# Kernel optimization log

Measured on AMD Instinct MI355X. Metric: run time of the kernel, lower is better.

## Reference

```python
import jax, jax.numpy as jnp
import numpy as np

# Model dims (see init_kwargs)
B, S = 4, 512
H = 1024            # hidden_size
I = 2816            # expert intermediate_size
E = 8               # num_experts
K = 2               # num_experts_per_tok
IS = 1408           # shared_expert_intermediate_size


def setup_inputs() -> dict:
    key = jax.random.key(0)
    ks = jax.random.split(key, 8)
    def init(k, shape, fan_in):
        return (jax.random.normal(k, shape, jnp.float32) / np.sqrt(fan_in)).astype(jnp.float32)
    return {
        "hidden_states": jax.random.normal(ks[0], (B, S, H), jnp.float32),
        "gate_w": init(ks[1], (H, E), H),          # router Linear (no bias)
        "Wg": init(ks[2], (E, H, I), H),           # per-expert gate_proj
        "Wu": init(ks[3], (E, H, I), H),           # per-expert up_proj
        "Wd": init(ks[4], (E, I, H), I),           # per-expert down_proj
        "Sg": init(ks[5], (H, IS), H),             # shared expert gate_proj
        "Su": init(ks[6], (H, IS), H),             # shared expert up_proj
        "Sd": init(ks[7], (IS, H), IS),            # shared expert down_proj
    }


def reference(hidden_states, gate_w, Wg, Wu, Wd, Sg, Su, Sd):
    b, s, h = hidden_states.shape
    x = hidden_states.reshape(-1, h)                       # [T, H]
    T = x.shape[0]

    # Router: top-k logits, softmax over selected logits only
    logits = x @ gate_w                                    # [T, E]
    top_v, top_i = jax.lax.top_k(logits, K)                # [T, K]
    top_p = jax.nn.softmax(top_v, axis=-1)                 # [T, K]

    # Dense combine weights: combine[t, e] = sum of probs of slots routed to e
    combine = jnp.zeros((T, E), x.dtype).at[
        jnp.arange(T)[:, None], top_i
    ].add(top_p)                                           # [T, E]

    # All-expert SwiGLU (dense, vectorized over experts), then weighted combine
    g = jnp.einsum('th,ehi->tei', x, Wg)                   # [T, E, I]
    u = jnp.einsum('th,ehi->tei', x, Wu)
    d = jnp.einsum('tei,eih->teh', jax.nn.silu(g) * u, Wd) # [T, E, H]
    expert_out = jnp.einsum('te,teh->th', combine, d)      # [T, H]

    # Shared expert (always active)
    shared = (jax.nn.silu(x @ Sg) * (x @ Su)) @ Sd         # [T, H]

    return (expert_out + shared).reshape(b, s, h)
```

## Files before the change

kernel.cpp:

```cpp
#include <hip/hip_runtime.h>
#include <hip/hip_bf16.h>

typedef __bf16 bf16;
typedef __bf16 bf16x4 __attribute__((ext_vector_type(4)));
typedef __bf16 bf16x8 __attribute__((ext_vector_type(8)));
typedef float f32x4 __attribute__((ext_vector_type(4)));

constexpr int T = 2048;
constexpr int HD = 1024;
constexpr int NE = 8;
constexpr int IEXP = 2816;
constexpr int ISH = 1408;
constexpr int NSLOT = T * 2;

typedef __attribute__((address_space(1))) void gvoid;
typedef __attribute__((address_space(3))) void svoid;

__device__ __forceinline__ void gload_lds16(const void* g, void* l) {
  __builtin_amdgcn_global_load_lds((gvoid*)g, (svoid*)l, 16, 0, 0);
}

__global__ __launch_bounds__(256) void k_convert_x(const float* __restrict__ x,
                                                   bf16* __restrict__ xb, int n4) {
  int i = blockIdx.x * blockDim.x + threadIdx.x;
  if (i >= n4) return;
  float4 v = reinterpret_cast<const float4*>(x)[i];
  bf16x4 o; o[0] = (bf16)v.x; o[1] = (bf16)v.y; o[2] = (bf16)v.z; o[3] = (bf16)v.w;
  reinterpret_cast<bf16x4*>(xb)[i] = o;
}

__global__ __launch_bounds__(256) void k_transpose(const float* __restrict__ in,
                                                   bf16* __restrict__ out,
                                                   int Kd, int Nd) {
  __shared__ float tile[32][33];
  int b = blockIdx.z;
  int n0 = blockIdx.x * 32, k0 = blockIdx.y * 32;
  const float* src = in + (size_t)b * Kd * Nd;
  bf16* dst = out + (size_t)b * Kd * Nd;
  int t = threadIdx.x;
  int r = t >> 3, c4 = (t & 7) * 4;
  float4 v = *reinterpret_cast<const float4*>(src + (size_t)(k0 + r) * Nd + n0 + c4);
  tile[r][c4 + 0] = v.x; tile[r][c4 + 1] = v.y; tile[r][c4 + 2] = v.z; tile[r][c4 + 3] = v.w;
  __syncthreads();
  bf16x4 o;
  o[0] = (bf16)tile[c4 + 0][r]; o[1] = (bf16)tile[c4 + 1][r];
  o[2] = (bf16)tile[c4 + 2][r]; o[3] = (bf16)tile[c4 + 3][r];
  *reinterpret_cast<bf16x4*>(dst + (size_t)(n0 + r) * Kd + k0 + c4) = o;
}

__global__ __launch_bounds__(64) void k_router(const float* __restrict__ x,
                                               const float* __restrict__ gw,
                                               int* __restrict__ topi,
                                               float* __restrict__ topp,
                                               int* __restrict__ counts) {
  int t = blockIdx.x;
  int l = threadIdx.x;
  float acc[NE];
  #pragma unroll
  for (int e = 0; e < NE; ++e) acc[e] = 0.f;
  const float* xr = x + (size_t)t * HD;
  for (int i = 0; i < HD / 64; ++i) {
    int h = i * 64 + l;
    float xv = xr[h];
    const float* g = gw + (size_t)h * NE;
    #pragma unroll
    for (int e = 0; e < NE; ++e) acc[e] += xv * g[e];
  }
  #pragma unroll
  for (int e = 0; e < NE; ++e) {
    float v = acc[e];
    #pragma unroll
    for (int s = 32; s; s >>= 1) v += __shfl_xor(v, s);
    acc[e] = v;
  }
  if (l == 0) {
    int i0 = 0; float v0 = acc[0];
    #pragma unroll
    for (int e = 1; e < NE; ++e) if (acc[e] > v0) { v0 = acc[e]; i0 = e; }
    int i1 = -1; float v1 = -1e30f;
    #pragma unroll
    for (int e = 0; e < NE; ++e) if (e != i0 && acc[e] > v1) { v1 = acc[e]; i1 = e; }
    float e1 = expf(v1 - v0);
    float den = 1.f + e1;
    topi[t * 2] = i0; topi[t * 2 + 1] = i1;
    topp[t * 2] = 1.f / den; topp[t * 2 + 1] = e1 / den;
    atomicAdd(&counts[i0], 1);
    atomicAdd(&counts[i1], 1);
  }
}

__global__ void k_scan(const int* __restrict__ counts, int* __restrict__ offs,
                       int* __restrict__ cursor, int* __restrict__ soffs) {
  if (threadIdx.x == 0 && blockIdx.x == 0) {
    int s = 0; offs[0] = 0;
    for (int e = 0; e < NE; ++e) { s += counts[e]; offs[e + 1] = s; cursor[e] = 0; }
    soffs[0] = 0; soffs[1] = T;
  }
}

__global__ __launch_bounds__(64) void k_scatter(const int* __restrict__ topi,
                                                const float* __restrict__ topp,
                                                const int* __restrict__ offs,
                                                int* __restrict__ cursor,
                                                int* __restrict__ rowmap,
                                                float* __restrict__ rowp,
                                                int* __restrict__ slotOf) {
  int t = blockIdx.x * blockDim.x + threadIdx.x;
  if (t >= T) return;
  #pragma unroll
  for (int s = 0; s < 2; ++s) {
    int e = topi[t * 2 + s];
    int pos = offs[e] + atomicAdd(&cursor[e], 1);
    rowmap[pos] = t;
    rowp[pos] = topp[t * 2 + s];
    slotOf[t * 2 + s] = pos;
  }
}

__global__ __launch_bounds__(256) void k_gateup(
    const bf16* __restrict__ A, const int* __restrict__ rowmap,
    const int* __restrict__ offs, const bf16* __restrict__ Bg,
    const bf16* __restrict__ Bu, bf16* __restrict__ outp, int Nd, int Kd) {
  __shared__ alignas(16) bf16 As[128 * 32];
  __shared__ alignas(16) bf16 Bgs[64 * 32];
  __shared__ alignas(16) bf16 Bus[64 * 32];
  const int z = blockIdx.z;
  const int r0 = offs[z], r1 = offs[z + 1];
  const int mbase = r0 + blockIdx.y * 128;
  if (mbase >= r1) return;
  const int n0 = blockIdx.x * 64;
  const int tid = threadIdx.x, wid = tid >> 6, lane = tid & 63;

  const bf16 *aSrc0, *aSrc1;
  {
    int rl0 = wid * 32 + (lane >> 2);
    int g0 = mbase + rl0;      if (g0 >= r1) g0 = r1 - 1;
    int g1 = mbase + rl0 + 16; if (g1 >= r1) g1 = r1 - 1;
    int s0 = rowmap ? rowmap[g0] : g0;
    int s1 = rowmap ? rowmap[g1] : g1;
    aSrc0 = A + (size_t)s0 * Kd + (lane & 3) * 8;
    aSrc1 = A + (size_t)s1 * Kd + (lane & 3) * 8;
  }
  const size_t bstride = (size_t)Nd * Kd;
  const size_t brow = (size_t)(n0 + wid * 16 + (lane >> 2)) * Kd + (lane & 3) * 8;
  const bf16* bgSrc = Bg + (size_t)z * bstride + brow;
  const bf16* buSrc = Bu + (size_t)z * bstride + brow;
  bf16* aDst0 = &As[(wid * 32) * 32];
  bf16* aDst1 = &As[(wid * 32 + 16) * 32];
  bf16* bgDst = &Bgs[(wid * 16) * 32];
  bf16* buDst = &Bus[(wid * 16) * 32];

  f32x4 zz = {0.f, 0.f, 0.f, 0.f};
  f32x4 accg[4][2], accu[4][2];
  #pragma unroll
  for (int m = 0; m < 4; ++m)
    #pragma unroll
    for (int n = 0; n < 2; ++n) { accg[m][n] = zz; accu[m][n] = zz; }

  const int wr = wid >> 1, wc = wid & 1;
  const int frow = lane & 15, fk = (lane >> 4) * 8;

  for (int k0 = 0; k0 < Kd; k0 += 32) {
    gload_lds16(aSrc0 + k0, aDst0);
    gload_lds16(aSrc1 + k0, aDst1);
    gload_lds16(bgSrc + k0, bgDst);
    gload_lds16(buSrc + k0, buDst);
    __syncthreads();
    bf16x8 af[4], bgf[2], buf2[2];
    #pragma unroll
    for (int m = 0; m < 4; ++m)
      af[m] = *reinterpret_cast<const bf16x8*>(&As[(wr * 64 + m * 16 + frow) * 32 + fk]);
    #pragma unroll
    for (int n = 0; n < 2; ++n) {
      bgf[n]  = *reinterpret_cast<const bf16x8*>(&Bgs[(wc * 32 + n * 16 + frow) * 32 + fk]);
      buf2[n] = *reinterpret_cast<const bf16x8*>(&Bus[(wc * 32 + n * 16 + frow) * 32 + fk]);
    }
    #pragma unroll
    for (int m = 0; m < 4; ++m)
      #pragma unroll
      for (int n = 0; n < 2; ++n) {
        accg[m][n] = __builtin_amdgcn_mfma_f32_16x16x32_bf16(af[m], bgf[n],  accg[m][n], 0, 0, 0);
        accu[m][n] = __builtin_amdgcn_mfma_f32_16x16x32_bf16(af[m], buf2[n], accu[m][n], 0, 0, 0);
      }
    __syncthreads();
  }

  #pragma unroll
  for (int m = 0; m < 4; ++m)
    #pragma unroll
    for (int n = 0; n < 2; ++n)
      #pragma unroll
      for (int j = 0; j < 4; ++j) {
        int r = mbase + wr * 64 + m * 16 + (lane >> 4) * 4 + j;
        if (r < r1) {
          int c = n0 + wc * 32 + n * 16 + (lane & 15);
          float g = accg[m][n][j], u = accu[m][n][j];
          float sv = g / (1.f + __expf(-g));
          outp[(size_t)r * Nd + c] = (bf16)(sv * u);
        }
      }
}

__global__ __launch_bounds__(256) void k_down(
    const bf16* __restrict__ A, const float* __restrict__ rowp,
    const int* __restrict__ offs, const bf16* __restrict__ Bt,
    float* __restrict__ outp, int Nd, int Kd) {
  __shared__ alignas(16) bf16 As[128 * 32];
  __shared__ alignas(16) bf16 Bs[128 * 32];
  const int z = blockIdx.z;
  const int r0 = offs[z], r1 = offs[z + 1];
  const int mbase = r0 + blockIdx.y * 128;
  if (mbase >= r1) return;
  const int n0 = blockIdx.x * 128;
  const int tid = threadIdx.x, wid = tid >> 6, lane = tid & 63;

  const bf16 *aSrc0, *aSrc1;
  {
    int rl0 = wid * 32 + (lane >> 2);
    int g0 = mbase + rl0;      if (g0 >= r1) g0 = r1 - 1;
    int g1 = mbase + rl0 + 16; if (g1 >= r1) g1 = r1 - 1;
    aSrc0 = A + (size_t)g0 * Kd + (lane & 3) * 8;
    aSrc1 = A + (size_t)g1 * Kd + (lane & 3) * 8;
  }
  const bf16* bSrc0 = Bt + (size_t)z * Nd * Kd +
                      (size_t)(n0 + wid * 32 + (lane >> 2)) * Kd + (lane & 3) * 8;
  const bf16* bSrc1 = bSrc0 + (size_t)16 * Kd;
  bf16* aDst0 = &As[(wid * 32) * 32];
  bf16* aDst1 = &As[(wid * 32 + 16) * 32];
  bf16* bDst0 = &Bs[(wid * 32) * 32];
  bf16* bDst1 = &Bs[(wid * 32 + 16) * 32];

  f32x4 zz = {0.f, 0.f, 0.f, 0.f};
  f32x4 acc[4][4];
  #pragma unroll
  for (int m = 0; m < 4; ++m)
    #pragma unroll
    for (int n = 0; n < 4; ++n) acc[m][n] = zz;

  const int wr = wid >> 1, wc = wid & 1;
  const int frow = lane & 15, fk = (lane >> 4) * 8;

  for (int k0 = 0; k0 < Kd; k0 += 32) {
    gload_lds16(aSrc0 + k0, aDst0);
    gload_lds16(aSrc1 + k0, aDst1);
    gload_lds16(bSrc0 + k0, bDst0);
    gload_lds16(bSrc1 + k0, bDst1);
    __syncthreads();
    bf16x8 af[4], bfr[4];
    #pragma unroll
    for (int m = 0; m < 4; ++m)
      af[m] = *reinterpret_cast<const bf16x8*>(&As[(wr * 64 + m * 16 + frow) * 32 + fk]);
    #pragma unroll
    for (int n = 0; n < 4; ++n)
      bfr[n] = *reinterpret_cast<const bf16x8*>(&Bs[(wc * 64 + n * 16 + frow) * 32 + fk]);
    #pragma unroll
    for (int m = 0; m < 4; ++m)
      #pragma unroll
      for (int n = 0; n < 4; ++n)
        acc[m][n] = __builtin_amdgcn_mfma_f32_16x16x32_bf16(af[m], bfr[n], acc[m][n], 0, 0, 0);
    __syncthreads();
  }

  #pragma unroll
  for (int m = 0; m < 4; ++m)
    #pragma unroll
    for (int j = 0; j < 4; ++j) {
      int r = mbase + wr * 64 + m * 16 + (lane >> 4) * 4 + j;
      if (r < r1) {
        float sc = rowp ? rowp[r] : 1.f;
        #pragma unroll
        for (int n = 0; n < 4; ++n) {
          int c = n0 + wc * 64 + n * 16 + (lane & 15);
          outp[(size_t)r * Nd + c] = sc * acc[m][n][j];
        }
      }
    }
}

__global__ __launch_bounds__(256) void k_combine(const float* __restrict__ dout,
                                                 const float* __restrict__ sdown,
                                                 const int* __restrict__ slotOf,
                                                 float* __restrict__ outp) {
  int i = blockIdx.x * blockDim.x + threadIdx.x;
  if (i >= T * HD / 4) return;
  int t = i >> 8;
  int off = (i & 255) * 4;
  int s0 = slotOf[t * 2], s1 = slotOf[t * 2 + 1];
  float4 a = *reinterpret_cast<const float4*>(dout + (size_t)s0 * HD + off);
  float4 b = *reinterpret_cast<const float4*>(dout + (size_t)s1 * HD + off);
  float4 c = *reinterpret_cast<const float4*>(sdown + (size_t)i * 4);
  float4 o;
  o.x = a.x + b.x + c.x; o.y = a.y + b.y + c.y;
  o.z = a.z + b.z + c.z; o.w = a.w + b.w + c.w;
  *reinterpret_cast<float4*>(outp + (size_t)i * 4) = o;
}

static inline size_t algn(size_t x) { return (x + 255) & ~(size_t)255; }

extern "C" void kernel_launch(void* const* d_in, const int* in_sizes, int n_in,
                              void* d_out, int out_size, void* d_ws, size_t ws_size,
                              hipStream_t stream) {
  const float* x  = (const float*)d_in[0];
  const float* gw = (const float*)d_in[1];
  const float* Wg = (const float*)d_in[2];
  const float* Wu = (const float*)d_in[3];
  const float* Wd = (const float*)d_in[4];
  const float* Sg = (const float*)d_in[5];
  const float* Su = (const float*)d_in[6];
  const float* Sd = (const float*)d_in[7];
  float* out = (float*)d_out;

  char* p = (char*)d_ws;
  auto carve = [&](size_t bytes) -> char* { char* r = p; p += algn(bytes); return r; };
  bf16* xb   = (bf16*)carve((size_t)T * HD * 2);
  bf16* WgT  = (bf16*)carve((size_t)NE * IEXP * HD * 2);
  bf16* WuT  = (bf16*)carve((size_t)NE * IEXP * HD * 2);
  bf16* WdT  = (bf16*)carve((size_t)NE * HD * IEXP * 2);
  bf16* SgT  = (bf16*)carve((size_t)ISH * HD * 2);
  bf16* SuT  = (bf16*)carve((size_t)ISH * HD * 2);
  bf16* SdT  = (bf16*)carve((size_t)HD * ISH * 2);
  bf16* act  = (bf16*)carve((size_t)NSLOT * IEXP * 2);
  bf16* sact = (bf16*)carve((size_t)T * ISH * 2);
  float* dout  = (float*)carve((size_t)NSLOT * HD * 4);
  float* sdown = (float*)carve((size_t)T * HD * 4);
  int*   topi   = (int*)carve(T * 2 * 4);
  float* topp   = (float*)carve(T * 2 * 4);
  int*   rowmap = (int*)carve(NSLOT * 4);
  float* rowp   = (float*)carve(NSLOT * 4);
  int*   slotOf = (int*)carve(T * 2 * 4);
  int*   counts = (int*)carve(NE * 4);
  int*   offs   = (int*)carve((NE + 1) * 4);
  int*   cursor = (int*)carve(NE * 4);
  int*   soffs  = (int*)carve(2 * 4);

  hipMemsetAsync(counts, 0, NE * sizeof(int), stream);

  k_convert_x<<<T * HD / 4 / 256, 256, 0, stream>>>(x, xb, T * HD / 4);

  k_transpose<<<dim3(IEXP / 32, HD / 32, NE), 256, 0, stream>>>(Wg, WgT, HD, IEXP);
  k_transpose<<<dim3(IEXP / 32, HD / 32, NE), 256, 0, stream>>>(Wu, WuT, HD, IEXP);
  k_transpose<<<dim3(HD / 32, IEXP / 32, NE), 256, 0, stream>>>(Wd, WdT, IEXP, HD);
  k_transpose<<<dim3(ISH / 32, HD / 32, 1), 256, 0, stream>>>(Sg, SgT, HD, ISH);
  k_transpose<<<dim3(ISH / 32, HD / 32, 1), 256, 0, stream>>>(Su, SuT, HD, ISH);
  k_transpose<<<dim3(HD / 32, ISH / 32, 1), 256, 0, stream>>>(Sd, SdT, ISH, HD);

  k_router<<<T, 64, 0, stream>>>(x, gw, topi, topp, counts);
  k_scan<<<1, 64, 0, stream>>>(counts, offs, cursor, soffs);
  k_scatter<<<T / 64, 64, 0, stream>>>(topi, topp, offs, cursor, rowmap, rowp, slotOf);

  k_gateup<<<dim3(IEXP / 64, 32, NE), 256, 0, stream>>>(xb, rowmap, offs, WgT, WuT,
                                                        act, IEXP, HD);
  k_gateup<<<dim3(ISH / 64, T / 128, 1), 256, 0, stream>>>(xb, nullptr, soffs, SgT, SuT,
                                                           sact, ISH, HD);
  k_down<<<dim3(HD / 128, 32, NE), 256, 0, stream>>>(act, rowp, offs, WdT, dout, HD, IEXP);
  k_down<<<dim3(HD / 128, T / 128, 1), 256, 0, stream>>>(sact, nullptr, soffs, SdT,
                                                         sdown, HD, ISH);

  k_combine<<<T * HD / 4 / 256, 256, 0, stream>>>(dout, sdown, slotOf, out);

  (void)in_sizes; (void)n_in; (void)out_size; (void)ws_size;
}
```

Baseline: 649.4 us.

## Use 64-wide K tiles with XOR-swizzled LDS, split-K merged down GEMM

```diff
diff --git a/kernel.cpp b/kernel.cpp
--- a/kernel.cpp
+++ b/kernel.cpp
@@ -29,23 +29,36 @@
   reinterpret_cast<bf16x4*>(xb)[i] = o;
 }
 
-__global__ __launch_bounds__(256) void k_transpose(const float* __restrict__ in,
-                                                   bf16* __restrict__ out,
-                                                   int Kd, int Nd) {
-  __shared__ float tile[32][33];
-  int b = blockIdx.z;
-  int n0 = blockIdx.x * 32, k0 = blockIdx.y * 32;
+__global__ __launch_bounds__(256) void k_transpose64(const float* __restrict__ in,
+                                                     bf16* __restrict__ out,
+                                                     int Kd, int Nd) {
+  __shared__ float tile[64][65];
+  const int b = blockIdx.z;
+  const int n0 = blockIdx.x * 64, k0 = blockIdx.y * 64;
   const float* src = in + (size_t)b * Kd * Nd;
   bf16* dst = out + (size_t)b * Kd * Nd;
-  int t = threadIdx.x;
-  int r = t >> 3, c4 = (t & 7) * 4;
-  float4 v = *reinterpret_cast<const float4*>(src + (size_t)(k0 + r) * Nd + n0 + c4);
-  tile[r][c4 + 0] = v.x; tile[r][c4 + 1] = v.y; tile[r][c4 + 2] = v.z; tile[r][c4 + 3] = v.w;
+  const int t = threadIdx.x;
+  {
+    const int r = t >> 4, c = (t & 15) * 4;
+    #pragma unroll
+    for (int p = 0; p < 4; ++p) {
+      float4 v = *reinterpret_cast<const float4*>(src + (size_t)(k0 + p * 16 + r) * Nd + n0 + c);
+      tile[p * 16 + r][c + 0] = v.x; tile[p * 16 + r][c + 1] = v.y;
+      tile[p * 16 + r][c + 2] = v.z; tile[p * 16 + r][c + 3] = v.w;
+    }
+  }
   __syncthreads();
-  bf16x4 o;
-  o[0] = (bf16)tile[c4 + 0][r]; o[1] = (bf16)tile[c4 + 1][r];
-  o[2] = (bf16)tile[c4 + 2][r]; o[3] = (bf16)tile[c4 + 3][r];
-  *reinterpret_cast<bf16x4*>(dst + (size_t)(n0 + r) * Kd + k0 + c4) = o;
+  {
+    const int kc = (t & 7) * 8;
+    #pragma unroll
+    for (int p = 0; p < 2; ++p) {
+      const int nr = p * 32 + (t >> 3);
+      bf16x8 o;
+      #pragma unroll
+      for (int j = 0; j < 8; ++j) o[j] = (bf16)tile[kc + j][nr];
+      *reinterpret_cast<bf16x8*>(dst + (size_t)(n0 + nr) * Kd + k0 + kc) = o;
+    }
+  }
 }
 
 __global__ __launch_bounds__(64) void k_router(const float* __restrict__ x,
@@ -121,9 +134,9 @@
     const bf16* __restrict__ A, const int* __restrict__ rowmap,
     const int* __restrict__ offs, const bf16* __restrict__ Bg,
     const bf16* __restrict__ Bu, bf16* __restrict__ outp, int Nd, int Kd) {
-  __shared__ alignas(16) bf16 As[128 * 32];
-  __shared__ alignas(16) bf16 Bgs[64 * 32];
-  __shared__ alignas(16) bf16 Bus[64 * 32];
+  __shared__ alignas(16) bf16 As[128 * 64];
+  __shared__ alignas(16) bf16 Bgs[64 * 64];
+  __shared__ alignas(16) bf16 Bus[64 * 64];
   const int z = blockIdx.z;
   const int r0 = offs[z], r1 = offs[z + 1];
   const int mbase = r0 + blockIdx.y * 128;
@@ -131,24 +144,31 @@
   const int n0 = blockIdx.x * 64;
   const int tid = threadIdx.x, wid = tid >> 6, lane = tid & 63;
 
-  const bf16 *aSrc0, *aSrc1;
-  {
-    int rl0 = wid * 32 + (lane >> 2);
-    int g0 = mbase + rl0;      if (g0 >= r1) g0 = r1 - 1;
-    int g1 = mbase + rl0 + 16; if (g1 >= r1) g1 = r1 - 1;
-    int s0 = rowmap ? rowmap[g0] : g0;
-    int s1 = rowmap ? rowmap[g1] : g1;
-    aSrc0 = A + (size_t)s0 * Kd + (lane & 3) * 8;
-    aSrc1 = A + (size_t)s1 * Kd + (lane & 3) * 8;
+  const int srow = tid >> 3;
+  const int ls = (tid & 7) ^ (srow & 7);
+  const bf16* aSrc[4];
+  #pragma unroll
+  for (int i = 0; i < 4; ++i) {
+    int row = i * 32 + srow;
+    int g = mbase + row; if (g >= r1) g = r1 - 1;
+    int s = rowmap ? rowmap[g] : g;
+    aSrc[i] = A + (size_t)s * Kd + ls * 8;
   }
   const size_t bstride = (size_t)Nd * Kd;
-  const size_t brow = (size_t)(n0 + wid * 16 + (lane >> 2)) * Kd + (lane & 3) * 8;
-  const bf16* bgSrc = Bg + (size_t)z * bstride + brow;
-  const bf16* buSrc = Bu + (size_t)z * bstride + brow;
-  bf16* aDst0 = &As[(wid * 32) * 32];
-  bf16* aDst1 = &As[(wid * 32 + 16) * 32];
-  bf16* bgDst = &Bgs[(wid * 16) * 32];
-  bf16* buDst = &Bus[(wid * 16) * 32];
+  const bf16 *bgSrc[2], *buSrc[2];
+  #pragma unroll
+  for (int i = 0; i < 2; ++i) {
+    int row = i * 32 + srow;
+    size_t off = (size_t)z * bstride + (size_t)(n0 + row) * Kd + ls * 8;
+    bgSrc[i] = Bg + off;
+    buSrc[i] = Bu + off;
+  }
+  bf16* aDst[4]; bf16* bgDst[2]; bf16* buDst[2];
+  #pragma unroll
+  for (int i = 0; i < 4; ++i) aDst[i] = &As[i * 2048 + wid * 512];
+  #pragma unroll
+  for (int i = 0; i < 2; ++i) { bgDst[i] = &Bgs[i * 2048 + wid * 512];
+                                buDst[i] = &Bus[i * 2048 + wid * 512]; }
 
   f32x4 zz = {0.f, 0.f, 0.f, 0.f};
   f32x4 accg[4][2], accu[4][2];
@@ -158,30 +178,35 @@
     for (int n = 0; n < 2; ++n) { accg[m][n] = zz; accu[m][n] = zz; }
 
   const int wr = wid >> 1, wc = wid & 1;
-  const int frow = lane & 15, fk = (lane >> 4) * 8;
-
-  for (int k0 = 0; k0 < Kd; k0 += 32) {
-    gload_lds16(aSrc0 + k0, aDst0);
-    gload_lds16(aSrc1 + k0, aDst1);
-    gload_lds16(bgSrc + k0, bgDst);
-    gload_lds16(buSrc + k0, buDst);
+  const int frow = lane & 15, x7 = frow & 7, khi = lane >> 4;
+
+  for (int k0 = 0; k0 < Kd; k0 += 64) {
+    #pragma unroll
+    for (int i = 0; i < 4; ++i) gload_lds16(aSrc[i] + k0, aDst[i]);
+    #pragma unroll
+    for (int i = 0; i < 2; ++i) { gload_lds16(bgSrc[i] + k0, bgDst[i]);
+                                  gload_lds16(buSrc[i] + k0, buDst[i]); }
     __syncthreads();
-    bf16x8 af[4], bgf[2], buf2[2];
-    #pragma unroll
-    for (int m = 0; m < 4; ++m)
-      af[m] = *reinterpret_cast<const bf16x8*>(&As[(wr * 64 + m * 16 + frow) * 32 + fk]);
-    #pragma unroll
-    for (int n = 0; n < 2; ++n) {
-      bgf[n]  = *reinterpret_cast<const bf16x8*>(&Bgs[(wc * 32 + n * 16 + frow) * 32 + fk]);
-      buf2[n] = *reinterpret_cast<const bf16x8*>(&Bus[(wc * 32 + n * 16 + frow) * 32 + fk]);
+    #pragma unroll
+    for (int s = 0; s < 2; ++s) {
+      const int phys = ((4 * s + khi) ^ x7) * 8;
+      bf16x8 af[4], bgf[2], buf2[2];
+      #pragma unroll
+      for (int m = 0; m < 4; ++m)
+        af[m] = *reinterpret_cast<const bf16x8*>(&As[(wr * 64 + m * 16 + frow) * 64 + phys]);
+      #pragma unroll
+      for (int n = 0; n < 2; ++n) {
+        bgf[n]  = *reinterpret_cast<const bf16x8*>(&Bgs[(wc * 32 + n * 16 + frow) * 64 + phys]);
+        buf2[n] = *reinterpret_cast<const bf16x8*>(&Bus[(wc * 32 + n * 16 + frow) * 64 + phys]);
+      }
+      #pragma unroll
+      for (int m = 0; m < 4; ++m)
+        #pragma unroll
+        for (int n = 0; n < 2; ++n) {
+          accg[m][n] = __builtin_amdgcn_mfma_f32_16x16x32_bf16(af[m], bgf[n],  accg[m][n], 0, 0, 0);
+          accu[m][n] = __builtin_amdgcn_mfma_f32_16x16x32_bf16(af[m], buf2[n], accu[m][n], 0, 0, 0);
+        }
     }
-    #pragma unroll
-    for (int m = 0; m < 4; ++m)
-      #pragma unroll
-      for (int n = 0; n < 2; ++n) {
-        accg[m][n] = __builtin_amdgcn_mfma_f32_16x16x32_bf16(af[m], bgf[n],  accg[m][n], 0, 0, 0);
-        accu[m][n] = __builtin_amdgcn_mfma_f32_16x16x32_bf16(af[m], buf2[n], accu[m][n], 0, 0, 0);
-      }
     __syncthreads();
   }
 
@@ -202,33 +227,45 @@
 }
 
 __global__ __launch_bounds__(256) void k_down(
-    const bf16* __restrict__ A, const float* __restrict__ rowp,
-    const int* __restrict__ offs, const bf16* __restrict__ Bt,
-    float* __restrict__ outp, int Nd, int Kd) {
-  __shared__ alignas(16) bf16 As[128 * 32];
-  __shared__ alignas(16) bf16 Bs[128 * 32];
+    const bf16* __restrict__ act, const bf16* __restrict__ sact,
+    const float* __restrict__ rowp, const int* __restrict__ offs,
+    const bf16* __restrict__ WdT, const bf16* __restrict__ SdT,
+    float* __restrict__ pd, float* __restrict__ ps) {
+  __shared__ alignas(16) bf16 Asm[128 * 64];
+  __shared__ alignas(16) bf16 Bsm[128 * 64];
   const int z = blockIdx.z;
-  const int r0 = offs[z], r1 = offs[z + 1];
+  const bf16* A; const bf16* Bt; const float* scale; float* outp;
+  int r0, r1, Kd, kbase, klen;
+  if (z < 16) {
+    int e = z >> 1, c = z & 1;
+    A = act; Bt = WdT + (size_t)e * HD * IEXP; scale = rowp;
+    outp = pd + (size_t)c * NSLOT * HD;
+    r0 = offs[e]; r1 = offs[e + 1]; Kd = IEXP; klen = IEXP / 2; kbase = c * klen;
+  } else {
+    int c = z - 16;
+    A = sact; Bt = SdT; scale = nullptr;
+    outp = ps + (size_t)c * T * HD;
+    r0 = 0; r1 = T; Kd = ISH; klen = ISH / 2; kbase = c * klen;
+  }
   const int mbase = r0 + blockIdx.y * 128;
   if (mbase >= r1) return;
   const int n0 = blockIdx.x * 128;
   const int tid = threadIdx.x, wid = tid >> 6, lane = tid & 63;
 
-  const bf16 *aSrc0, *aSrc1;
-  {
-    int rl0 = wid * 32 + (lane >> 2);
-    int g0 = mbase + rl0;      if (g0 >= r1) g0 = r1 - 1;
-    int g1 = mbase + rl0 + 16; if (g1 >= r1) g1 = r1 - 1;
-    aSrc0 = A + (size_t)g0 * Kd + (lane & 3) * 8;
-    aSrc1 = A + (size_t)g1 * Kd + (lane & 3) * 8;
-  }
-  const bf16* bSrc0 = Bt + (size_t)z * Nd * Kd +
-                      (size_t)(n0 + wid * 32 + (lane >> 2)) * Kd + (lane & 3) * 8;
-  const bf16* bSrc1 = bSrc0 + (size_t)16 * Kd;
-  bf16* aDst0 = &As[(wid * 32) * 32];
-  bf16* aDst1 = &As[(wid * 32 + 16) * 32];
-  bf16* bDst0 = &Bs[(wid * 32) * 32];
-  bf16* bDst1 = &Bs[(wid * 32 + 16) * 32];
+  const int srow = tid >> 3;
+  const int ls = (tid & 7) ^ (srow & 7);
+  const bf16* aSrc[4]; const bf16* bSrc[4];
+  #pragma unroll
+  for (int i = 0; i < 4; ++i) {
+    int row = i * 32 + srow;
+    int g = mbase + row; if (g >= r1) g = r1 - 1;
+    aSrc[i] = A + (size_t)g * Kd + kbase + ls * 8;
+    bSrc[i] = Bt + (size_t)(n0 + row) * Kd + kbase + ls * 8;
+  }
+  bf16* aDst[4]; bf16* bDst[4];
+  #pragma unroll
+  for (int i = 0; i < 4; ++i) { aDst[i] = &Asm[i * 2048 + wid * 512];
+                                bDst[i] = &Bsm[i * 2048 + wid * 512]; }
 
   f32x4 zz = {0.f, 0.f, 0.f, 0.f};
   f32x4 acc[4][4];
@@ -238,26 +275,29 @@
     for (int n = 0; n < 4; ++n) acc[m][n] = zz;
 
   const int wr = wid >> 1, wc = wid & 1;
-  const int frow = lane & 15, fk = (lane >> 4) * 8;
-
-  for (int k0 = 0; k0 < Kd; k0 += 32) {
-    gload_lds16(aSrc0 + k0, aDst0);
-    gload_lds16(aSrc1 + k0, aDst1);
-    gload_lds16(bSrc0 + k0, bDst0);
-    gload_lds16(bSrc1 + k0, bDst1);
+  const int frow = lane & 15, x7 = frow & 7, khi = lane >> 4;
+
+  for (int k0 = 0; k0 < klen; k0 += 64) {
+    #pragma unroll
+    for (int i = 0; i < 4; ++i) { gload_lds16(aSrc[i] + k0, aDst[i]);
+                                  gload_lds16(bSrc[i] + k0, bDst[i]); }
     __syncthreads();
-    bf16x8 af[4], bfr[4];
-    #pragma unroll
-    for (int m = 0; m < 4; ++m)
-      af[m] = *reinterpret_cast<const bf16x8*>(&As[(wr * 64 + m * 16 + frow) * 32 + fk]);
-    #pragma unroll
-    for (int n = 0; n < 4; ++n)
-      bfr[n] = *reinterpret_cast<const bf16x8*>(&Bs[(wc * 64 + n * 16 + frow) * 32 + fk]);
-    #pragma unroll
-    for (int m = 0; m < 4; ++m)
+    #pragma unroll
+    for (int s = 0; s < 2; ++s) {
+      const int phys = ((4 * s + khi) ^ x7) * 8;
+      bf16x8 af[4], bfr[4];
+      #pragma unroll
+      for (int m = 0; m < 4; ++m)
+        af[m] = *reinterpret_cast<const bf16x8*>(&Asm[(wr * 64 + m * 16 + frow) * 64 + phys]);
       #pragma unroll
       for (int n = 0; n < 4; ++n)
-        acc[m][n] = __builtin_amdgcn_mfma_f32_16x16x32_bf16(af[m], bfr[n], acc[m][n], 0, 0, 0);
+        bfr[n] = *reinterpret_cast<const bf16x8*>(&Bsm[(wc * 64 + n * 16 + frow) * 64 + phys]);
+      #pragma unroll
+      for (int m = 0; m < 4; ++m)
+        #pragma unroll
+        for (int n = 0; n < 4; ++n)
+          acc[m][n] = __builtin_amdgcn_mfma_f32_16x16x32_bf16(af[m], bfr[n], acc[m][n], 0, 0, 0);
+    }
     __syncthreads();
   }
 
@@ -267,18 +307,18 @@
     for (int j = 0; j < 4; ++j) {
       int r = mbase + wr * 64 + m * 16 + (lane >> 4) * 4 + j;
       if (r < r1) {
-        float sc = rowp ? rowp[r] : 1.f;
+        float sc = scale ? scale[r] : 1.f;
         #pragma unroll
         for (int n = 0; n < 4; ++n) {
           int c = n0 + wc * 64 + n * 16 + (lane & 15);
-          outp[(size_t)r * Nd + c] = sc * acc[m][n][j];
+          outp[(size_t)r * HD + c] = sc * acc[m][n][j];
         }
       }
     }
 }
 
-__global__ __launch_bounds__(256) void k_combine(const float* __restrict__ dout,
-                                                 const float* __restrict__ sdown,
+__global__ __launch_bounds__(256) void k_combine(const float* __restrict__ pd,
+                                                 const float* __restrict__ ps,
                                                  const int* __restrict__ slotOf,
                                                  float* __restrict__ outp) {
   int i = blockIdx.x * blockDim.x + threadIdx.x;
@@ -286,12 +326,19 @@
   int t = i >> 8;
   int off = (i & 255) * 4;
   int s0 = slotOf[t * 2], s1 = slotOf[t * 2 + 1];
-  float4 a = *reinterpret_cast<const float4*>(dout + (size_t)s0 * HD + off);
-  float4 b = *reinterpret_cast<const float4*>(dout + (size_t)s1 * HD + off);
-  float4 c = *reinterpret_cast<const float4*>(sdown + (size_t)i * 4);
+  const float* pd1 = pd + (size_t)NSLOT * HD;
+  const float* ps1 = ps + (size_t)T * HD;
+  float4 a0 = *reinterpret_cast<const float4*>(pd  + (size_t)s0 * HD + off);
+  float4 a1 = *reinterpret_cast<const float4*>(pd1 + (size_t)s0 * HD + off);
+  float4 b0 = *reinterpret_cast<const float4*>(pd  + (size_t)s1 * HD + off);
+  float4 b1 = *reinterpret_cast<const float4*>(pd1 + (size_t)s1 * HD + off);
+  float4 c0 = *reinterpret_cast<const float4*>(ps  + (size_t)i * 4);
+  float4 c1 = *reinterpret_cast<const float4*>(ps1 + (size_t)i * 4);
   float4 o;
-  o.x = a.x + b.x + c.x; o.y = a.y + b.y + c.y;
-  o.z = a.z + b.z + c.z; o.w = a.w + b.w + c.w;
+  o.x = a0.x + a1.x + b0.x + b1.x + c0.x + c1.x;
+  o.y = a0.y + a1.y + b0.y + b1.y + c0.y + c1.y;
+  o.z = a0.z + a1.z + b0.z + b1.z + c0.z + c1.z;
+  o.w = a0.w + a1.w + b0.w + b1.w + c0.w + c1.w;
   *reinterpret_cast<float4*>(outp + (size_t)i * 4) = o;
 }
 
@@ -321,8 +368,8 @@
   bf16* SdT  = (bf16*)carve((size_t)HD * ISH * 2);
   bf16* act  = (bf16*)carve((size_t)NSLOT * IEXP * 2);
   bf16* sact = (bf16*)carve((size_t)T * ISH * 2);
-  float* dout  = (float*)carve((size_t)NSLOT * HD * 4);
-  float* sdown = (float*)carve((size_t)T * HD * 4);
+  float* pd  = (float*)carve((size_t)2 * NSLOT * HD * 4);
+  float* ps  = (float*)carve((size_t)2 * T * HD * 4);
   int*   topi   = (int*)carve(T * 2 * 4);
   float* topp   = (float*)carve(T * 2 * 4);
   int*   rowmap = (int*)carve(NSLOT * 4);
@@ -337,26 +384,25 @@
 
   k_convert_x<<<T * HD / 4 / 256, 256, 0, stream>>>(x, xb, T * HD / 4);
 
-  k_transpose<<<dim3(IEXP / 32, HD / 32, NE), 256, 0, stream>>>(Wg, WgT, HD, IEXP);
-  k_transpose<<<dim3(IEXP / 32, HD / 32, NE), 256, 0, stream>>>(Wu, WuT, HD, IEXP);
-  k_transpose<<<dim3(HD / 32, IEXP / 32, NE), 256, 0, stream>>>(Wd, WdT, IEXP, HD);
-  k_transpose<<<dim3(ISH / 32, HD / 32, 1), 256, 0, stream>>>(Sg, SgT, HD, ISH);
-  k_transpose<<<dim3(ISH / 32, HD / 32, 1), 256, 0, stream>>>(Su, SuT, HD, ISH);
-  k_transpose<<<dim3(HD / 32, ISH / 32, 1), 256, 0, stream>>>(Sd, SdT, ISH, HD);
+  k_transpose64<<<dim3(IEXP / 64, HD / 64, NE), 256, 0, stream>>>(Wg, WgT, HD, IEXP);
+  k_transpose64<<<dim3(IEXP / 64, HD / 64, NE), 256, 0, stream>>>(Wu, WuT, HD, IEXP);
+  k_transpose64<<<dim3(HD / 64, IEXP / 64, NE), 256, 0, stream>>>(Wd, WdT, IEXP, HD);
+  k_transpose64<<<dim3(ISH / 64, HD / 64, 1), 256, 0, stream>>>(Sg, SgT, HD, ISH);
+  k_transpose64<<<dim3(ISH / 64, HD / 64, 1), 256, 0, stream>>>(Su, SuT, HD, ISH);
+  k_transpose64<<<dim3(HD / 64, ISH / 64, 1), 256, 0, stream>>>(Sd, SdT, ISH, HD);
 
   k_router<<<T, 64, 0, stream>>>(x, gw, topi, topp, counts);
   k_scan<<<1, 64, 0, stream>>>(counts, offs, cursor, soffs);
   k_scatter<<<T / 64, 64, 0, stream>>>(topi, topp, offs, cursor, rowmap, rowp, slotOf);
 
-  k_gateup<<<dim3(IEXP / 64, 32, NE), 256, 0, stream>>>(xb, rowmap, offs, WgT, WuT,
+  k_gateup<<<dim3(IEXP / 64, 16, NE), 256, 0, stream>>>(xb, rowmap, offs, WgT, WuT,
                                                         act, IEXP, HD);
   k_gateup<<<dim3(ISH / 64, T / 128, 1), 256, 0, stream>>>(xb, nullptr, soffs, SgT, SuT,
                                                            sact, ISH, HD);
-  k_down<<<dim3(HD / 128, 32, NE), 256, 0, stream>>>(act, rowp, offs, WdT, dout, HD, IEXP);
-  k_down<<<dim3(HD / 128, T / 128, 1), 256, 0, stream>>>(sact, nullptr, soffs, SdT,
-                                                         sdown, HD, ISH);
-
-  k_combine<<<T * HD / 4 / 256, 256, 0, stream>>>(dout, sdown, slotOf, out);
+  k_down<<<dim3(HD / 128, 16, 18), 256, 0, stream>>>(act, sact, rowp, offs, WdT, SdT,
+                                                     pd, ps);
+
+  k_combine<<<T * HD / 4 / 256, 256, 0, stream>>>(pd, ps, slotOf, out);
 
   (void)in_sizes; (void)n_in; (void)out_size; (void)ws_size;
 }
```

After: 560.1 us. -13.7%, faster.
